# Optimization experiments

Measured on AMD Instinct MI355X. Metric: run time of the kernel, lower is better.

The kernel has to match this reference:

```python
import jax, jax.numpy as jnp
import numpy as np

BATCH, SEQ, D_MODEL = 4, 4096, 2048
DSTATE, N_HEADS = 64, 16
D_INNER = DSTATE * N_HEADS  # 1024, must equal d_mamba


def setup_inputs() -> dict:
    key = jax.random.key(0)
    ks = jax.random.split(key, 6)
    x_norm = jax.random.normal(ks[0], (BATCH, SEQ, D_MODEL), jnp.float32)
    inv = 1.0 / np.sqrt(D_MODEL)
    Wx = jax.random.normal(ks[1], (D_INNER, D_MODEL), jnp.float32) * inv
    # dt_proj: weight std 0.001, bias -4.0 (as in module init)
    Wdt = jax.random.normal(ks[2], (D_INNER, D_MODEL), jnp.float32) * 0.001
    b_dt = jnp.full((D_INNER,), -4.0, jnp.float32)
    WB = jax.random.normal(ks[3], (DSTATE, D_MODEL), jnp.float32) * inv
    WC = jax.random.normal(ks[4], (DSTATE, D_MODEL), jnp.float32) * inv
    A_log = jnp.tile(jnp.log(jnp.arange(1, DSTATE + 1, dtype=jnp.float32))[None, :], (N_HEADS, 1))
    Dp = jnp.ones((D_INNER,), jnp.float32)
    Wout = jax.random.normal(ks[5], (D_INNER, D_INNER), jnp.float32) * (1.0 / np.sqrt(D_INNER))
    return {"x_norm": x_norm, "Wx": Wx, "Wdt": Wdt, "b_dt": b_dt,
            "WB": WB, "WC": WC, "A_log": A_log, "Dp": Dp, "Wout": Wout}


def reference(x_norm, Wx, Wdt, b_dt, WB, WC, A_log, Dp, Wout):
    # projections
    x_ssm = jnp.einsum("btd,id->bti", x_norm, Wx)                       # (B,T,D_inner)
    dt = jax.nn.softplus(jnp.einsum("btd,id->bti", x_norm, Wdt) + b_dt)
    dt = jnp.clip(dt, 1e-4, 0.5)
    Bm = jnp.einsum("btd,nd->btn", x_norm, WB)                          # (B,T,N)
    Cm = jnp.einsum("btd,nd->btn", x_norm, WC)
    Bm = Bm / jnp.maximum(jnp.linalg.norm(Bm, axis=-1, keepdims=True), 1.0)
    Cm = Cm / jnp.maximum(jnp.linalg.norm(Cm, axis=-1, keepdims=True), 1.0)
    # discretized diagonal SSM: h_t = dA_t * h_{t-1} + dt_t * B_t * x_t
    A_neg = -jnp.exp(A_log.reshape(-1))                                  # (D_inner,)
    dA = jnp.exp(dt * A_neg)                                             # (B,T,D_inner)
    B_exp = jnp.tile(Bm, (1, 1, N_HEADS))                                # repeat across heads
    C_exp = jnp.tile(Cm, (1, 1, N_HEADS))
    dBx = dt * B_exp * x_ssm

    def combine(c1, c2):
        a1, b1 = c1
        a2, b2 = c2
        return a2 * a1, a2 * b1 + b2

    _, h = jax.lax.associative_scan(combine, (dA, dBx), axis=1)          # (B,T,D_inner)
    y = C_exp * h + Dp * x_ssm
    return jnp.einsum("bti,oi->bto", y, Wout)
```

## Files before the change

### kernel.cpp

```cpp
#include <hip/hip_runtime.h>
#include <hip/hip_bf16.h>
#include <math.h>

#define BATCH  4
#define SEQ    4096
#define DMODEL 2048
#define DSTATE 64
#define DINNER 1024
#define MTOT   (BATCH*SEQ)
#define NPROJ  (DINNER+DINNER+DSTATE+DSTATE)
#define CH     128
#define NC     (SEQ/CH)

typedef __attribute__((ext_vector_type(8))) short bf16x8;
typedef __attribute__((ext_vector_type(4))) float f32x4;

__device__ __forceinline__ unsigned short f2bf(float v) {
    __hip_bfloat16 b = __float2bfloat16(v);
    unsigned short u; __builtin_memcpy(&u, &b, 2); return u;
}
__device__ __forceinline__ float bf2f(unsigned short u) {
    __hip_bfloat16 b; __builtin_memcpy(&b, &u, 2); return __bfloat162float(b);
}
__device__ __forceinline__ void split2(float v, unsigned short& h, unsigned short& l) {
    h = f2bf(v);
    l = f2bf(v - bf2f(h));
}

__device__ __forceinline__ bf16x8 frag_ld(const unsigned short* buf, int row, int lg) {
    int j = lg ^ ((row >> 1) & 3);
    return *reinterpret_cast<const bf16x8*>(&buf[row * 32 + j * 8]);
}

__global__ __launch_bounds__(256, 2)
void proj_gemm(const float* __restrict__ X,
               const unsigned short* __restrict__ Wh,
               const unsigned short* __restrict__ Wl,
               const float* __restrict__ b_dt,
               float* __restrict__ x_ssm, float* __restrict__ dt,
               float* __restrict__ Bm,    float* __restrict__ Cm)
{
    __shared__ unsigned short Ahs[128*32];
    __shared__ unsigned short Als[128*32];
    __shared__ unsigned short Bhs[128*32];
    __shared__ unsigned short Bls[128*32];

    const int tid  = threadIdx.x;
    const int lane = tid & 63;
    const int w    = tid >> 6;
    const int wr   = (w >> 1) * 64;
    const int wc   = (w & 1)  * 64;
    const int l15  = lane & 15;
    const int lg   = lane >> 4;

    const int nwg   = gridDim.x * gridDim.y;
    const int bid   = blockIdx.y * gridDim.x + blockIdx.x;
    const int swz   = (bid & 7) * (nwg >> 3) + (bid >> 3);
    const int nblk  = (swz % gridDim.x) * 128;
    const int mblk  = (swz / gridDim.x) * 128;

    f32x4 acc[4][4];
    #pragma unroll
    for (int m = 0; m < 4; ++m)
        #pragma unroll
        for (int n = 0; n < 4; ++n)
            acc[m][n] = (f32x4){0.f, 0.f, 0.f, 0.f};

    for (int k0 = 0; k0 < DMODEL; k0 += 32) {
        float4 av[4];
        #pragma unroll
        for (int r = 0; r < 4; ++r) {
            int s   = r * 256 + tid;
            int row = s >> 3, seg = s & 7;
            av[r] = *reinterpret_cast<const float4*>(
                &X[(size_t)(mblk + row) * DMODEL + k0 + seg * 4]);
        }
        __syncthreads();
        #pragma unroll
        for (int r = 0; r < 4; ++r) {
            int s   = r * 256 + tid;
            int row = s >> 3, seg = s & 7;
            int off = row * 32 + (((seg >> 1) ^ ((row >> 1) & 3)) * 8) + (seg & 1) * 4;
            unsigned short h0,h1,h2,h3,l0,l1,l2,l3;
            split2(av[r].x, h0, l0); split2(av[r].y, h1, l1);
            split2(av[r].z, h2, l2); split2(av[r].w, h3, l3);
            *reinterpret_cast<ushort4*>(&Ahs[off]) = make_ushort4(h0,h1,h2,h3);
            *reinterpret_cast<ushort4*>(&Als[off]) = make_ushort4(l0,l1,l2,l3);
        }
        #pragma unroll
        for (int r = 0; r < 2; ++r) {
            int s    = r * 256 + tid;
            int row  = s >> 2, j = s & 3;
            int js   = j ^ ((row >> 1) & 3);
            const unsigned short* srch = &Wh[(size_t)(nblk + row) * DMODEL + k0 + js * 8];
            const unsigned short* srcl = &Wl[(size_t)(nblk + row) * DMODEL + k0 + js * 8];
            unsigned short* dsth = &Bhs[(size_t)(r * 256 + w * 64) * 8];
            unsigned short* dstl = &Bls[(size_t)(r * 256 + w * 64) * 8];
            __builtin_amdgcn_global_load_lds(
                (const __attribute__((address_space(1))) void*)srch,
                (__attribute__((address_space(3))) void*)dsth, 16, 0, 0);
            __builtin_amdgcn_global_load_lds(
                (const __attribute__((address_space(1))) void*)srcl,
                (__attribute__((address_space(3))) void*)dstl, 16, 0, 0);
        }
        __syncthreads();

        bf16x8 af[4][2], bfr[4][2];
        #pragma unroll
        for (int m = 0; m < 4; ++m) {
            int row = wr + m * 16 + l15;
            af[m][0] = frag_ld(Ahs, row, lg);
            af[m][1] = frag_ld(Als, row, lg);
        }
        #pragma unroll
        for (int n = 0; n < 4; ++n) {
            int row = wc + n * 16 + l15;
            bfr[n][0] = frag_ld(Bhs, row, lg);
            bfr[n][1] = frag_ld(Bls, row, lg);
        }
        #pragma unroll
        for (int m = 0; m < 4; ++m)
            #pragma unroll
            for (int n = 0; n < 4; ++n) {
                acc[m][n] = __builtin_amdgcn_mfma_f32_16x16x32_bf16(af[m][0], bfr[n][0], acc[m][n], 0, 0, 0);
                acc[m][n] = __builtin_amdgcn_mfma_f32_16x16x32_bf16(af[m][0], bfr[n][1], acc[m][n], 0, 0, 0);
                acc[m][n] = __builtin_amdgcn_mfma_f32_16x16x32_bf16(af[m][1], bfr[n][0], acc[m][n], 0, 0, 0);
            }
    }

    #pragma unroll
    for (int m = 0; m < 4; ++m) {
        #pragma unroll
        for (int n = 0; n < 4; ++n) {
            int gn = nblk + wc + n * 16 + l15;
            float bv = (gn >= 1024 && gn < 2048) ? b_dt[gn - 1024] : 0.0f;
            #pragma unroll
            for (int q = 0; q < 4; ++q) {
                int gm = mblk + wr + m * 16 + lg * 4 + q;
                float v = acc[m][n][q];
                if (gn < 1024) {
                    x_ssm[(size_t)gm * DINNER + gn] = v;
                } else if (gn < 2048) {
                    float z  = v + bv;
                    float sp = z > 15.f ? z : log1pf(expf(z));
                    dt[(size_t)gm * DINNER + (gn - 1024)] =
                        fminf(fmaxf(sp, 1e-4f), 0.5f);
                } else if (gn < 2112) {
                    Bm[(size_t)gm * DSTATE + (gn - 2048)] = v;
                } else {
                    Cm[(size_t)gm * DSTATE + (gn - 2112)] = v;
                }
            }
        }
    }
}

__global__ __launch_bounds__(256, 2)
void out_gemm(const unsigned short* __restrict__ Yh, const unsigned short* __restrict__ Yl,
              const unsigned short* __restrict__ Woh, const unsigned short* __restrict__ Wol,
              float* __restrict__ Out)
{
    __shared__ unsigned short Ahs[128*32];
    __shared__ unsigned short Als[128*32];
    __shared__ unsigned short Bhs[128*32];
    __shared__ unsigned short Bls[128*32];

    const int tid  = threadIdx.x;
    const int lane = tid & 63;
    const int w    = tid >> 6;
    const int wr   = (w >> 1) * 64;
    const int wc   = (w & 1)  * 64;
    const int l15  = lane & 15;
    const int lg   = lane >> 4;

    const int nwg   = gridDim.x * gridDim.y;
    const int bid   = blockIdx.y * gridDim.x + blockIdx.x;
    const int swz   = (bid & 7) * (nwg >> 3) + (bid >> 3);
    const int nblk  = (swz % gridDim.x) * 128;
    const int mblk  = (swz / gridDim.x) * 128;

    f32x4 acc[4][4];
    #pragma unroll
    for (int m = 0; m < 4; ++m)
        #pragma unroll
        for (int n = 0; n < 4; ++n)
            acc[m][n] = (f32x4){0.f, 0.f, 0.f, 0.f};

    for (int k0 = 0; k0 < DINNER; k0 += 32) {
        __syncthreads();
        #pragma unroll
        for (int r = 0; r < 2; ++r) {
            int s    = r * 256 + tid;
            int row  = s >> 2, j = s & 3;
            int js   = j ^ ((row >> 1) & 3);
            size_t aoff = (size_t)(mblk + row) * DINNER + k0 + js * 8;
            size_t boff = (size_t)(nblk + row) * DINNER + k0 + js * 8;
            unsigned short* da_h = &Ahs[(size_t)(r * 256 + w * 64) * 8];
            unsigned short* da_l = &Als[(size_t)(r * 256 + w * 64) * 8];
            unsigned short* db_h = &Bhs[(size_t)(r * 256 + w * 64) * 8];
            unsigned short* db_l = &Bls[(size_t)(r * 256 + w * 64) * 8];
            __builtin_amdgcn_global_load_lds(
                (const __attribute__((address_space(1))) void*)&Yh[aoff],
                (__attribute__((address_space(3))) void*)da_h, 16, 0, 0);
            __builtin_amdgcn_global_load_lds(
                (const __attribute__((address_space(1))) void*)&Yl[aoff],
                (__attribute__((address_space(3))) void*)da_l, 16, 0, 0);
            __builtin_amdgcn_global_load_lds(
                (const __attribute__((address_space(1))) void*)&Woh[boff],
                (__attribute__((address_space(3))) void*)db_h, 16, 0, 0);
            __builtin_amdgcn_global_load_lds(
                (const __attribute__((address_space(1))) void*)&Wol[boff],
                (__attribute__((address_space(3))) void*)db_l, 16, 0, 0);
        }
        __syncthreads();

        bf16x8 af[4][2], bfr[4][2];
        #pragma unroll
        for (int m = 0; m < 4; ++m) {
            int row = wr + m * 16 + l15;
            af[m][0] = frag_ld(Ahs, row, lg);
            af[m][1] = frag_ld(Als, row, lg);
        }
        #pragma unroll
        for (int n = 0; n < 4; ++n) {
            int row = wc + n * 16 + l15;
            bfr[n][0] = frag_ld(Bhs, row, lg);
            bfr[n][1] = frag_ld(Bls, row, lg);
        }
        #pragma unroll
        for (int m = 0; m < 4; ++m)
            #pragma unroll
            for (int n = 0; n < 4; ++n) {
                acc[m][n] = __builtin_amdgcn_mfma_f32_16x16x32_bf16(af[m][0], bfr[n][0], acc[m][n], 0, 0, 0);
                acc[m][n] = __builtin_amdgcn_mfma_f32_16x16x32_bf16(af[m][0], bfr[n][1], acc[m][n], 0, 0, 0);
                acc[m][n] = __builtin_amdgcn_mfma_f32_16x16x32_bf16(af[m][1], bfr[n][0], acc[m][n], 0, 0, 0);
            }
    }

    #pragma unroll
    for (int m = 0; m < 4; ++m) {
        #pragma unroll
        for (int n = 0; n < 4; ++n) {
            #pragma unroll
            for (int q = 0; q < 4; ++q) {
                size_t gm = mblk + wr + m * 16 + lg * 4 + q;
                int    gn = nblk + wc + n * 16 + l15;
                Out[gm * DINNER + gn] = acc[m][n][q];
            }
        }
    }
}

__global__ void split_f32(const float* __restrict__ src, unsigned short* __restrict__ h,
                          unsigned short* __restrict__ l, int n4)
{
    int stride = gridDim.x * blockDim.x;
    for (int i = blockIdx.x * blockDim.x + threadIdx.x; i < n4; i += stride) {
        float4 v = reinterpret_cast<const float4*>(src)[i];
        unsigned short h0,h1,h2,h3,l0,l1,l2,l3;
        split2(v.x, h0, l0); split2(v.y, h1, l1);
        split2(v.z, h2, l2); split2(v.w, h3, l3);
        reinterpret_cast<ushort4*>(h)[i] = make_ushort4(h0,h1,h2,h3);
        reinterpret_cast<ushort4*>(l)[i] = make_ushort4(l0,l1,l2,l3);
    }
}

__global__ void normalize_bc(float* __restrict__ Bm, float* __restrict__ Cm)
{
    int w    = (blockIdx.x * blockDim.x + threadIdx.x) >> 6;
    int lane = threadIdx.x & 63;
    int row  = w >> 1;
    float* M = (w & 1) ? Cm : Bm;
    float v = M[(size_t)row * DSTATE + lane];
    float s = v * v;
    #pragma unroll
    for (int off = 32; off; off >>= 1) s += __shfl_xor(s, off);
    float scale = 1.0f / fmaxf(sqrtf(s), 1.0f);
    M[(size_t)row * DSTATE + lane] = v * scale;
}

__global__ void scan_passA(const float* __restrict__ dt, const float* __restrict__ x_ssm,
                           const float* __restrict__ Bm, const float* __restrict__ A_log,
                           float* __restrict__ Asum, float* __restrict__ Psum)
{
    int bi = blockIdx.x;
    int ib = bi & 3;
    int c  = (bi >> 2) & (NC - 1);
    int b  = bi >> 7;
    int i  = ib * 256 + threadIdx.x;
    float aneg = -expf(A_log[i]);
    float Aacc = 1.0f, P = 0.0f;
    size_t rowbase = (size_t)b * SEQ + (size_t)c * CH;
    for (int t = 0; t < CH; ++t) {
        size_t off = (rowbase + t) * DINNER + i;
        float d  = dt[off];
        float x  = x_ssm[off];
        float Bv = Bm[(rowbase + t) * DSTATE + (i & 63)];
        float a  = expf(d * aneg);
        Aacc *= a;
        P = fmaf(a, P, d * Bv * x);
    }
    size_t so = ((size_t)b * NC + c) * DINNER + i;
    Asum[so] = Aacc; Psum[so] = P;
}

__global__ void scan_chunkprefix(const float* __restrict__ Asum,
                                 const float* __restrict__ Psum,
                                 float* __restrict__ H)
{
    int idx = blockIdx.x * blockDim.x + threadIdx.x;
    int b = idx >> 10, i = idx & 1023;
    float h = 0.0f;
    for (int c = 0; c < NC; ++c) {
        size_t so = ((size_t)b * NC + c) * DINNER + i;
        H[so] = h;
        h = fmaf(Asum[so], h, Psum[so]);
    }
}

__global__ void scan_passB(const float* __restrict__ dt, const float* __restrict__ x_ssm,
                           const float* __restrict__ Bm, const float* __restrict__ Cm,
                           const float* __restrict__ A_log, const float* __restrict__ Dp,
                           const float* __restrict__ H,
                           unsigned short* __restrict__ Yh, unsigned short* __restrict__ Yl)
{
    int bi = blockIdx.x;
    int ib = bi & 3;
    int c  = (bi >> 2) & (NC - 1);
    int b  = bi >> 7;
    int i  = ib * 256 + threadIdx.x;
    float aneg = -expf(A_log[i]);
    float Dpi  = Dp[i];
    size_t so = ((size_t)b * NC + c) * DINNER + i;
    float h = H[so];
    size_t rowbase = (size_t)b * SEQ + (size_t)c * CH;
    for (int t = 0; t < CH; ++t) {
        size_t off = (rowbase + t) * DINNER + i;
        float d  = dt[off];
        float x  = x_ssm[off];
        float Bv = Bm[(rowbase + t) * DSTATE + (i & 63)];
        float Cv = Cm[(rowbase + t) * DSTATE + (i & 63)];
        float a  = expf(d * aneg);
        h = fmaf(a, h, d * Bv * x);
        float y = Cv * h + Dpi * x;
        unsigned short yh, yl;
        split2(y, yh, yl);
        Yh[off] = yh; Yl[off] = yl;
    }
}

extern "C" void kernel_launch(void* const* d_in, const int* in_sizes, int n_in,
                              void* d_out, int out_size, void* d_ws, size_t ws_size,
                              hipStream_t stream)
{
    const float* x_norm = (const float*)d_in[0];
    const float* Wx     = (const float*)d_in[1];
    const float* Wdt    = (const float*)d_in[2];
    const float* b_dt   = (const float*)d_in[3];
    const float* WB     = (const float*)d_in[4];
    const float* WC     = (const float*)d_in[5];
    const float* A_log  = (const float*)d_in[6];
    const float* Dp     = (const float*)d_in[7];
    const float* Wout   = (const float*)d_in[8];
    float* out = (float*)d_out;

    const size_t MB = 1024 * 1024;
    char* ws = (char*)d_ws;
    float* x_ssm = (float*)(ws);
    float* dtbuf = (float*)(ws + 64*MB);
    float* Bm    = (float*)(ws + 128*MB);
    float* Cm    = (float*)(ws + 132*MB);
    float* Asum  = (float*)(ws + 136*MB);
    float* Psum  = (float*)(ws + 136*MB + 512*1024);
    float* Hbuf  = (float*)(ws + 137*MB);
    unsigned short* Wh  = (unsigned short*)(ws + 138*MB);
    unsigned short* Wl  = (unsigned short*)(ws + 147*MB);
    unsigned short* Woh = (unsigned short*)(ws + 156*MB);
    unsigned short* Wol = (unsigned short*)(ws + 158*MB);
    unsigned short* Yh  = (unsigned short*)(ws + 160*MB);
    unsigned short* Yl  = (unsigned short*)(ws + 192*MB);

    const size_t WXN = (size_t)DINNER * DMODEL;
    const size_t WBN = (size_t)DSTATE * DMODEL;

    split_f32<<<1024, 256, 0, stream>>>(Wx,  Wh,             Wl,             (int)(WXN/4));
    split_f32<<<1024, 256, 0, stream>>>(Wdt, Wh + WXN,       Wl + WXN,       (int)(WXN/4));
    split_f32<<<64,   256, 0, stream>>>(WB,  Wh + 2*WXN,     Wl + 2*WXN,     (int)(WBN/4));
    split_f32<<<64,   256, 0, stream>>>(WC,  Wh + 2*WXN+WBN, Wl + 2*WXN+WBN, (int)(WBN/4));
    split_f32<<<1024, 256, 0, stream>>>(Wout, Woh, Wol, (int)((size_t)DINNER*DINNER/4));

    proj_gemm<<<dim3(NPROJ/128, MTOT/128), 256, 0, stream>>>(
        x_norm, Wh, Wl, b_dt, x_ssm, dtbuf, Bm, Cm);
    normalize_bc<<<(MTOT*2)/4, 256, 0, stream>>>(Bm, Cm);
    scan_passA<<<BATCH*NC*(DINNER/256), 256, 0, stream>>>(
        dtbuf, x_ssm, Bm, A_log, Asum, Psum);
    scan_chunkprefix<<<(BATCH*DINNER)/256, 256, 0, stream>>>(Asum, Psum, Hbuf);
    scan_passB<<<BATCH*NC*(DINNER/256), 256, 0, stream>>>(
        dtbuf, x_ssm, Bm, Cm, A_log, Dp, Hbuf, Yh, Yl);
    out_gemm<<<dim3(DINNER/128, MTOT/128), 256, 0, stream>>>(
        Yh, Yl, Woh, Wol, out);
}
```

Before: 899.6 us.

## Double-buffer LDS tiles in projection and output GEMMs to overlap loads with MFMA

Both GEMM kernels now keep two LDS tile sets (64KB total) and prefetch the next K-slice, through direct global-to-LDS loads and register-held X values, while MFMAs run on the current slice. This removes one barrier per iteration and hides global load latency behind compute. In exchange, LDS use doubles, which may limit occupancy to two blocks per CU (consistent with launch bounds) and adds register pressure from holding prefetched X values.

```diff
diff --git a/kernel.cpp b/kernel.cpp
--- a/kernel.cpp
+++ b/kernel.cpp
@@ -32,6 +32,54 @@
     return *reinterpret_cast<const bf16x8*>(&buf[row * 32 + j * 8]);
 }
 
+__device__ __forceinline__ void load_a(float4* av, const float* __restrict__ X,
+                                       int mblk, int k0, int tid)
+{
+#pragma unroll
+    for (int r = 0; r < 4; ++r) {
+        int s = r * 256 + tid;
+        int row = s >> 3, seg = s & 7;
+        av[r] = *reinterpret_cast<const float4*>(
+            &X[(size_t)(mblk + row) * DMODEL + k0 + seg * 4]);
+    }
+}
+
+__device__ __forceinline__ void stage_w(unsigned short (*dst)[4096],
+    const unsigned short* __restrict__ Wh, const unsigned short* __restrict__ Wl,
+    int nblk, int k0, int tid, int w)
+{
+#pragma unroll
+    for (int r = 0; r < 2; ++r) {
+        int s = r * 256 + tid;
+        int row = s >> 2, j = s & 3;
+        int js = j ^ ((row >> 1) & 3);
+        size_t o = (size_t)(nblk + row) * DMODEL + k0 + js * 8;
+        size_t d = (size_t)(r * 256 + w * 64) * 8;
+        __builtin_amdgcn_global_load_lds(
+            (const __attribute__((address_space(1))) void*)&Wh[o],
+            (__attribute__((address_space(3))) void*)&dst[2][d], 16, 0, 0);
+        __builtin_amdgcn_global_load_lds(
+            (const __attribute__((address_space(1))) void*)&Wl[o],
+            (__attribute__((address_space(3))) void*)&dst[3][d], 16, 0, 0);
+    }
+}
+
+__device__ __forceinline__ void write_a(unsigned short (*dst)[4096],
+                                        const float4* av, int tid)
+{
+#pragma unroll
+    for (int r = 0; r < 4; ++r) {
+        int s = r * 256 + tid;
+        int row = s >> 3, seg = s & 7;
+        int off = row * 32 + (((seg >> 1) ^ ((row >> 1) & 3)) * 8) + (seg & 1) * 4;
+        unsigned short h0,h1,h2,h3,l0,l1,l2,l3;
+        split2(av[r].x, h0, l0); split2(av[r].y, h1, l1);
+        split2(av[r].z, h2, l2); split2(av[r].w, h3, l3);
+        *reinterpret_cast<ushort4*>(&dst[0][off]) = make_ushort4(h0,h1,h2,h3);
+        *reinterpret_cast<ushort4*>(&dst[1][off]) = make_ushort4(l0,l1,l2,l3);
+    }
+}
+
 __global__ __launch_bounds__(256, 2)
 void proj_gemm(const float* __restrict__ X,
                const unsigned short* __restrict__ Wh,
@@ -40,10 +88,7 @@
                float* __restrict__ x_ssm, float* __restrict__ dt,
                float* __restrict__ Bm,    float* __restrict__ Cm)
 {
-    __shared__ unsigned short Ahs[128*32];
-    __shared__ unsigned short Als[128*32];
-    __shared__ unsigned short Bhs[128*32];
-    __shared__ unsigned short Bls[128*32];
+    __shared__ unsigned short sbuf[2][4][4096];
 
     const int tid  = threadIdx.x;
     const int lane = tid & 63;
@@ -53,11 +98,11 @@
     const int l15  = lane & 15;
     const int lg   = lane >> 4;
 
-    const int nwg   = gridDim.x * gridDim.y;
-    const int bid   = blockIdx.y * gridDim.x + blockIdx.x;
-    const int swz   = (bid & 7) * (nwg >> 3) + (bid >> 3);
-    const int nblk  = (swz % gridDim.x) * 128;
-    const int mblk  = (swz / gridDim.x) * 128;
+    const int nwg  = gridDim.x * gridDim.y;
+    const int bid  = blockIdx.y * gridDim.x + blockIdx.x;
+    const int swz  = (bid & 7) * (nwg >> 3) + (bid >> 3);
+    const int nblk = (swz % gridDim.x) * 128;
+    const int mblk = (swz / gridDim.x) * 128;
 
     f32x4 acc[4][4];
     #pragma unroll
@@ -66,66 +111,46 @@
         for (int n = 0; n < 4; ++n)
             acc[m][n] = (f32x4){0.f, 0.f, 0.f, 0.f};
 
-    for (int k0 = 0; k0 < DMODEL; k0 += 32) {
-        float4 av[4];
-        #pragma unroll
-        for (int r = 0; r < 4; ++r) {
-            int s   = r * 256 + tid;
-            int row = s >> 3, seg = s & 7;
-            av[r] = *reinterpret_cast<const float4*>(
-                &X[(size_t)(mblk + row) * DMODEL + k0 + seg * 4]);
-        }
-        __syncthreads();
-        #pragma unroll
-        for (int r = 0; r < 4; ++r) {
-            int s   = r * 256 + tid;
-            int row = s >> 3, seg = s & 7;
-            int off = row * 32 + (((seg >> 1) ^ ((row >> 1) & 3)) * 8) + (seg & 1) * 4;
-            unsigned short h0,h1,h2,h3,l0,l1,l2,l3;
-            split2(av[r].x, h0, l0); split2(av[r].y, h1, l1);
-            split2(av[r].z, h2, l2); split2(av[r].w, h3, l3);
-            *reinterpret_cast<ushort4*>(&Ahs[off]) = make_ushort4(h0,h1,h2,h3);
-            *reinterpret_cast<ushort4*>(&Als[off]) = make_ushort4(l0,l1,l2,l3);
-        }
-        #pragma unroll
-        for (int r = 0; r < 2; ++r) {
-            int s    = r * 256 + tid;
-            int row  = s >> 2, j = s & 3;
-            int js   = j ^ ((row >> 1) & 3);
-            const unsigned short* srch = &Wh[(size_t)(nblk + row) * DMODEL + k0 + js * 8];
-            const unsigned short* srcl = &Wl[(size_t)(nblk + row) * DMODEL + k0 + js * 8];
-            unsigned short* dsth = &Bhs[(size_t)(r * 256 + w * 64) * 8];
-            unsigned short* dstl = &Bls[(size_t)(r * 256 + w * 64) * 8];
-            __builtin_amdgcn_global_load_lds(
-                (const __attribute__((address_space(1))) void*)srch,
-                (__attribute__((address_space(3))) void*)dsth, 16, 0, 0);
-            __builtin_amdgcn_global_load_lds(
-                (const __attribute__((address_space(1))) void*)srcl,
-                (__attribute__((address_space(3))) void*)dstl, 16, 0, 0);
-        }
-        __syncthreads();
-
-        bf16x8 af[4][2], bfr[4][2];
+    float4 av[4];
+    load_a(av, X, mblk, 0, tid);
+    stage_w(sbuf[0], Wh, Wl, nblk, 0, tid, w);
+    write_a(sbuf[0], av, tid);
+    __syncthreads();
+
+    const int NT = DMODEL / 32;
+    int cur = 0;
+    for (int t = 0; t < NT; ++t) {
+        const bool pf = (t + 1 < NT);
+        if (pf) {
+            load_a(av, X, mblk, (t + 1) * 32, tid);
+            stage_w(sbuf[cur ^ 1], Wh, Wl, nblk, (t + 1) * 32, tid, w);
+        }
+
+        bf16x8 afh[4], afl[4], bfh[4], bfl[4];
         #pragma unroll
         for (int m = 0; m < 4; ++m) {
             int row = wr + m * 16 + l15;
-            af[m][0] = frag_ld(Ahs, row, lg);
-            af[m][1] = frag_ld(Als, row, lg);
+            afh[m] = frag_ld(sbuf[cur][0], row, lg);
+            afl[m] = frag_ld(sbuf[cur][1], row, lg);
         }
         #pragma unroll
         for (int n = 0; n < 4; ++n) {
             int row = wc + n * 16 + l15;
-            bfr[n][0] = frag_ld(Bhs, row, lg);
-            bfr[n][1] = frag_ld(Bls, row, lg);
+            bfh[n] = frag_ld(sbuf[cur][2], row, lg);
+            bfl[n] = frag_ld(sbuf[cur][3], row, lg);
         }
         #pragma unroll
         for (int m = 0; m < 4; ++m)
             #pragma unroll
             for (int n = 0; n < 4; ++n) {
-                acc[m][n] = __builtin_amdgcn_mfma_f32_16x16x32_bf16(af[m][0], bfr[n][0], acc[m][n], 0, 0, 0);
-                acc[m][n] = __builtin_amdgcn_mfma_f32_16x16x32_bf16(af[m][0], bfr[n][1], acc[m][n], 0, 0, 0);
-                acc[m][n] = __builtin_amdgcn_mfma_f32_16x16x32_bf16(af[m][1], bfr[n][0], acc[m][n], 0, 0, 0);
+                acc[m][n] = __builtin_amdgcn_mfma_f32_16x16x32_bf16(afh[m], bfh[n], acc[m][n], 0, 0, 0);
+                acc[m][n] = __builtin_amdgcn_mfma_f32_16x16x32_bf16(afh[m], bfl[n], acc[m][n], 0, 0, 0);
+                acc[m][n] = __builtin_amdgcn_mfma_f32_16x16x32_bf16(afl[m], bfh[n], acc[m][n], 0, 0, 0);
             }
+
+        if (pf) write_a(sbuf[cur ^ 1], av, tid);
+        __syncthreads();
+        cur ^= 1;
     }
 
     #pragma unroll
@@ -155,15 +180,40 @@
     }
 }
 
+__device__ __forceinline__ void stage4o(unsigned short (*dst)[4096],
+    const unsigned short* __restrict__ Ah, const unsigned short* __restrict__ Al,
+    const unsigned short* __restrict__ Bh, const unsigned short* __restrict__ Bl,
+    int mblk, int nblk, int k0, int tid, int w)
+{
+#pragma unroll
+    for (int r = 0; r < 2; ++r) {
+        int s   = r * 256 + tid;
+        int row = s >> 2, j = s & 3;
+        int js  = j ^ ((row >> 1) & 3);
+        size_t ao = (size_t)(mblk + row) * DINNER + k0 + js * 8;
+        size_t bo = (size_t)(nblk + row) * DINNER + k0 + js * 8;
+        size_t d  = (size_t)(r * 256 + w * 64) * 8;
+        __builtin_amdgcn_global_load_lds(
+            (const __attribute__((address_space(1))) void*)&Ah[ao],
+            (__attribute__((address_space(3))) void*)&dst[0][d], 16, 0, 0);
+        __builtin_amdgcn_global_load_lds(
+            (const __attribute__((address_space(1))) void*)&Al[ao],
+            (__attribute__((address_space(3))) void*)&dst[1][d], 16, 0, 0);
+        __builtin_amdgcn_global_load_lds(
+            (const __attribute__((address_space(1))) void*)&Bh[bo],
+            (__attribute__((address_space(3))) void*)&dst[2][d], 16, 0, 0);
+        __builtin_amdgcn_global_load_lds(
+            (const __attribute__((address_space(1))) void*)&Bl[bo],
+            (__attribute__((address_space(3))) void*)&dst[3][d], 16, 0, 0);
+    }
+}
+
 __global__ __launch_bounds__(256, 2)
 void out_gemm(const unsigned short* __restrict__ Yh, const unsigned short* __restrict__ Yl,
               const unsigned short* __restrict__ Woh, const unsigned short* __restrict__ Wol,
               float* __restrict__ Out)
 {
-    __shared__ unsigned short Ahs[128*32];
-    __shared__ unsigned short Als[128*32];
-    __shared__ unsigned short Bhs[128*32];
-    __shared__ unsigned short Bls[128*32];
+    __shared__ unsigned short sbuf[2][4][4096];
 
     const int tid  = threadIdx.x;
     const int lane = tid & 63;
@@ -173,11 +223,11 @@
     const int l15  = lane & 15;
     const int lg   = lane >> 4;
 
-    const int nwg   = gridDim.x * gridDim.y;
-    const int bid   = blockIdx.y * gridDim.x + blockIdx.x;
-    const int swz   = (bid & 7) * (nwg >> 3) + (bid >> 3);
-    const int nblk  = (swz % gridDim.x) * 128;
-    const int mblk  = (swz / gridDim.x) * 128;
+    const int nwg  = gridDim.x * gridDim.y;
+    const int bid  = blockIdx.y * gridDim.x + blockIdx.x;
+    const int swz  = (bid & 7) * (nwg >> 3) + (bid >> 3);
+    const int nblk = (swz % gridDim.x) * 128;
+    const int mblk = (swz / gridDim.x) * 128;
 
     f32x4 acc[4][4];
     #pragma unroll
@@ -186,55 +236,39 @@
         for (int n = 0; n < 4; ++n)
             acc[m][n] = (f32x4){0.f, 0.f, 0.f, 0.f};
 
-    for (int k0 = 0; k0 < DINNER; k0 += 32) {
-        __syncthreads();
-        #pragma unroll
-        for (int r = 0; r < 2; ++r) {
-            int s    = r * 256 + tid;
-            int row  = s >> 2, j = s & 3;
-            int js   = j ^ ((row >> 1) & 3);
-            size_t aoff = (size_t)(mblk + row) * DINNER + k0 + js * 8;
-            size_t boff = (size_t)(nblk + row) * DINNER + k0 + js * 8;
-            unsigned short* da_h = &Ahs[(size_t)(r * 256 + w * 64) * 8];
-            unsigned short* da_l = &Als[(size_t)(r * 256 + w * 64) * 8];
-            unsigned short* db_h = &Bhs[(size_t)(r * 256 + w * 64) * 8];
-            unsigned short* db_l = &Bls[(size_t)(r * 256 + w * 64) * 8];
-            __builtin_amdgcn_global_load_lds(
-                (const __attribute__((address_space(1))) void*)&Yh[aoff],
-                (__attribute__((address_space(3))) void*)da_h, 16, 0, 0);
-            __builtin_amdgcn_global_load_lds(
-                (const __attribute__((address_space(1))) void*)&Yl[aoff],
-                (__attribute__((address_space(3))) void*)da_l, 16, 0, 0);
-            __builtin_amdgcn_global_load_lds(
-                (const __attribute__((address_space(1))) void*)&Woh[boff],
-                (__attribute__((address_space(3))) void*)db_h, 16, 0, 0);
-            __builtin_amdgcn_global_load_lds(
-                (const __attribute__((address_space(1))) void*)&Wol[boff],
-                (__attribute__((address_space(3))) void*)db_l, 16, 0, 0);
-        }
-        __syncthreads();
-
-        bf16x8 af[4][2], bfr[4][2];
+    stage4o(sbuf[0], Yh, Yl, Woh, Wol, mblk, nblk, 0, tid, w);
+    __syncthreads();
+
+    const int NT = DINNER / 32;
+    int cur = 0;
+    for (int t = 0; t < NT; ++t) {
+        if (t + 1 < NT)
+            stage4o(sbuf[cur ^ 1], Yh, Yl, Woh, Wol, mblk, nblk, (t + 1) * 32, tid, w);
+
+        bf16x8 afh[4], afl[4], bfh[4], bfl[4];
         #pragma unroll
         for (int m = 0; m < 4; ++m) {
             int row = wr + m * 16 + l15;
-            af[m][0] = frag_ld(Ahs, row, lg);
-            af[m][1] = frag_ld(Als, row, lg);
+            afh[m] = frag_ld(sbuf[cur][0], row, lg);
+            afl[m] = frag_ld(sbuf[cur][1], row, lg);
         }
         #pragma unroll
         for (int n = 0; n < 4; ++n) {
             int row = wc + n * 16 + l15;
-            bfr[n][0] = frag_ld(Bhs, row, lg);
-            bfr[n][1] = frag_ld(Bls, row, lg);
+            bfh[n] = frag_ld(sbuf[cur][2], row, lg);
+            bfl[n] = frag_ld(sbuf[cur][3], row, lg);
         }
         #pragma unroll
         for (int m = 0; m < 4; ++m)
             #pragma unroll
             for (int n = 0; n < 4; ++n) {
-                acc[m][n] = __builtin_amdgcn_mfma_f32_16x16x32_bf16(af[m][0], bfr[n][0], acc[m][n], 0, 0, 0);
-                acc[m][n] = __builtin_amdgcn_mfma_f32_16x16x32_bf16(af[m][0], bfr[n][1], acc[m][n], 0, 0, 0);
-                acc[m][n] = __builtin_amdgcn_mfma_f32_16x16x32_bf16(af[m][1], bfr[n][0], acc[m][n], 0, 0, 0);
+                acc[m][n] = __builtin_amdgcn_mfma_f32_16x16x32_bf16(afh[m], bfh[n], acc[m][n], 0, 0, 0);
+                acc[m][n] = __builtin_amdgcn_mfma_f32_16x16x32_bf16(afh[m], bfl[n], acc[m][n], 0, 0, 0);
+                acc[m][n] = __builtin_amdgcn_mfma_f32_16x16x32_bf16(afl[m], bfh[n], acc[m][n], 0, 0, 0);
             }
+
+        __syncthreads();
+        cur ^= 1;
     }
 
     #pragma unroll
```

Result: slower. 949.8 us (+5.6%).
